# Performance work log

Measured on AMD Instinct MI355X. Metric: run time of the kernel, lower is better.

## Reference

```python
import jax, jax.numpy as jnp
import numpy as np

N_HEAD = 16
N_KV = 4
HEAD_DIM = 128
EPS = 1e-6


def setup_inputs() -> dict:
    key = jax.random.key(0)
    k1, k2, k3 = jax.random.split(key, 3)
    d_model = N_HEAD * HEAD_DIM
    qkv_out = (N_HEAD + 2 * N_KV) * HEAD_DIM
    B, T = 2, 2048
    x = jax.random.normal(k1, (B, T, d_model), dtype=jnp.float32)
    W_qkv = jax.random.normal(k2, (d_model, qkv_out), dtype=jnp.float32) * (d_model ** -0.5)
    W_proj = jax.random.normal(k3, (d_model, d_model), dtype=jnp.float32) * (d_model ** -0.5)
    q_scale = jnp.ones((HEAD_DIM,), dtype=jnp.float32)
    k_scale = jnp.ones((HEAD_DIM,), dtype=jnp.float32)
    return {"x": x, "W_qkv": W_qkv, "W_proj": W_proj, "q_scale": q_scale, "k_scale": k_scale}


def _rms_norm(t):
    return t * jax.lax.rsqrt(jnp.mean(t * t, axis=-1, keepdims=True) + EPS)


def reference(x, W_qkv, W_proj, q_scale, k_scale):
    B, T, C = x.shape
    qkv = x @ W_qkv  # [B, T, (H+2*KV)*D]
    q, k, v = jnp.split(qkv, [N_HEAD * HEAD_DIM, (N_HEAD + N_KV) * HEAD_DIM], axis=-1)
    q = q.reshape(B, T, N_HEAD, HEAD_DIM).transpose(0, 2, 1, 3)  # [B,H,T,D]
    k = k.reshape(B, T, N_KV, HEAD_DIM).transpose(0, 2, 1, 3)    # [B,KV,T,D]
    v = v.reshape(B, T, N_KV, HEAD_DIM).transpose(0, 2, 1, 3)
    # QK RMS-norm with learned per-dim scales
    q = _rms_norm(q) * q_scale
    k = _rms_norm(k) * k_scale
    # GQA: repeat kv heads to match query heads
    rep = N_HEAD // N_KV
    k = jnp.repeat(k, rep, axis=1)
    v = jnp.repeat(v, rep, axis=1)
    # causal SDPA
    scale = 1.0 / jnp.sqrt(jnp.float32(HEAD_DIM))
    scores = jnp.einsum('bhqd,bhkd->bhqk', q, k) * scale
    causal = jnp.tril(jnp.ones((T, T), dtype=bool))
    scores = jnp.where(causal, scores, jnp.finfo(scores.dtype).min)
    attn = jax.nn.softmax(scores, axis=-1)
    y = jnp.einsum('bhqk,bhkd->bhqd', attn, v)  # [B,H,T,D]
    y = y.transpose(0, 2, 1, 3).reshape(B, T, C)
    return y @ W_proj
```

## Files before the change

kernel.cpp:

```cpp
#include <hip/hip_runtime.h>

typedef __bf16 bf16;
typedef __bf16 bf16x8 __attribute__((ext_vector_type(8)));
typedef __bf16 bf16x4 __attribute__((ext_vector_type(4)));
typedef float f32x4 __attribute__((ext_vector_type(4)));
typedef float f32x16 __attribute__((ext_vector_type(16)));
typedef unsigned u32x4 __attribute__((ext_vector_type(4)));

#define EXP2F(x) __builtin_amdgcn_exp2f(x)

#define LOAD_LDS16(gp, lp)                                                     \
  __builtin_amdgcn_global_load_lds(                                            \
      (const __attribute__((address_space(1))) void*)(gp),                     \
      (__attribute__((address_space(3))) void*)(lp), 16, 0, 0)

__global__ __launch_bounds__(256) void k_cvt_x(const float* __restrict__ in,
                                               bf16* __restrict__ out, int n4) {
  int i = blockIdx.x * 256 + threadIdx.x;
  if (i < n4) {
    float4 v = ((const float4*)in)[i];
    bf16x4 o = {(bf16)v.x, (bf16)v.y, (bf16)v.z, (bf16)v.w};
    ((bf16x4*)out)[i] = o;
  }
}

__global__ __launch_bounds__(256) void k_transpose(const float* __restrict__ in,
                                                   bf16* __restrict__ out,
                                                   int R, int C) {
  __shared__ bf16 t[64 * 65];
  int tid = threadIdx.x;
  int c0 = blockIdx.x * 64, r0 = blockIdx.y * 64;
#pragma unroll
  for (int i = 0; i < 16; ++i) {
    int f = i * 256 + tid;
    int rl = f >> 6, cl = f & 63;
    t[rl * 65 + cl] = (bf16)in[(size_t)(r0 + rl) * C + c0 + cl];
  }
  __syncthreads();
#pragma unroll
  for (int i = 0; i < 16; ++i) {
    int f = i * 256 + tid;
    int cl = f >> 6, rl = f & 63;
    out[(size_t)(c0 + cl) * R + r0 + rl] = t[rl * 65 + cl];
  }
}

template <typename OutT>
__global__ __launch_bounds__(512, 2) void k_gemm256(const bf16* __restrict__ A,
                                                    const bf16* __restrict__ Bt,
                                                    OutT* __restrict__ C,
                                                    int M, int N, int K) {
  __shared__ alignas(16) bf16 As[2][2][4 * 256 * 8];
  __shared__ alignas(16) bf16 Bs[2][2][4 * 256 * 8];
  int tid = threadIdx.x;
  int wid = tid >> 6, lane = tid & 63;
  int g = lane >> 4, lr = lane & 15;
  int wrow = (wid >> 2) * 128, wcol = (wid & 3) * 64;
  int row0 = blockIdx.x * 256, col0 = blockIdx.y * 256;
  int NT = K >> 6;
  f32x4 acc[8][4] = {};

  auto stageA = [&](int buf, int kh, int kt) {
#pragma unroll
    for (int pass = 0; pass < 2; ++pass) {
      int slot = pass * 512 + tid;
      int kseg = slot >> 8, row = slot & 255;
      LOAD_LDS16(A + (size_t)(row0 + row) * K + kt * 64 + kh * 32 + kseg * 8,
                 &As[buf][kh][slot * 8]);
    }
  };
  auto stageB = [&](int buf, int kh, int kt) {
#pragma unroll
    for (int pass = 0; pass < 2; ++pass) {
      int slot = pass * 512 + tid;
      int kseg = slot >> 8, row = slot & 255;
      LOAD_LDS16(Bt + (size_t)(col0 + row) * K + kt * 64 + kh * 32 + kseg * 8,
                 &Bs[buf][kh][slot * 8]);
    }
  };
  auto dsA = [&](int buf, int s, int mq, bf16x8* af) {
#pragma unroll
    for (int i = 0; i < 4; ++i)
      af[i] = *(const bf16x8*)&As[buf][s]
                  [((g << 8) + wrow + (mq * 4 + i) * 16 + lr) * 8];
  };
  auto dsB = [&](int buf, int s, bf16x8* bfr) {
#pragma unroll
    for (int i = 0; i < 4; ++i)
      bfr[i] = *(const bf16x8*)&Bs[buf][s][((g << 8) + wcol + i * 16 + lr) * 8];
  };
  auto mfma16 = [&](int mq, bf16x8* af, bf16x8* bfr) {
    __builtin_amdgcn_s_setprio(1);
#pragma unroll
    for (int i = 0; i < 4; ++i)
#pragma unroll
      for (int n = 0; n < 4; ++n)
        acc[mq * 4 + i][n] = __builtin_amdgcn_mfma_f32_16x16x32_bf16(
            af[i], bfr[n], acc[mq * 4 + i][n], 0, 0, 0);
    __builtin_amdgcn_s_setprio(0);
  };

  stageA(0, 0, 0);
  stageB(0, 0, 0);
  stageA(0, 1, 0);
  stageB(0, 1, 0);
  asm volatile("s_waitcnt vmcnt(4)" ::: "memory");
  __builtin_amdgcn_s_barrier();

  for (int T = 0; T < NT; ++T) {
    int buf = T & 1, nbuf = buf ^ 1;
    bool more = (T + 1 < NT);
    bf16x8 af[4], bfr[4];
    dsA(buf, 0, 0, af);
    dsB(buf, 0, bfr);
    if (more) stageA(nbuf, 0, T + 1);
    __builtin_amdgcn_sched_barrier(0);
    __builtin_amdgcn_s_barrier();
    asm volatile("s_waitcnt lgkmcnt(0)" ::: "memory");
    __builtin_amdgcn_sched_barrier(0);
    mfma16(0, af, bfr);
    __builtin_amdgcn_s_barrier();
    dsA(buf, 0, 1, af);
    if (more) {
      stageB(nbuf, 0, T + 1);
      asm volatile("s_waitcnt vmcnt(4)" ::: "memory");
    } else {
      asm volatile("s_waitcnt vmcnt(0)" ::: "memory");
    }
    __builtin_amdgcn_sched_barrier(0);
    __builtin_amdgcn_s_barrier();
    asm volatile("s_waitcnt lgkmcnt(0)" ::: "memory");
    __builtin_amdgcn_sched_barrier(0);
    mfma16(1, af, bfr);
    __builtin_amdgcn_s_barrier();
    dsA(buf, 1, 0, af);
    dsB(buf, 1, bfr);
    if (more) stageA(nbuf, 1, T + 1);
    __builtin_amdgcn_sched_barrier(0);
    __builtin_amdgcn_s_barrier();
    asm volatile("s_waitcnt lgkmcnt(0)" ::: "memory");
    __builtin_amdgcn_sched_barrier(0);
    mfma16(0, af, bfr);
    __builtin_amdgcn_s_barrier();
    dsA(buf, 1, 1, af);
    if (more) {
      stageB(nbuf, 1, T + 1);
      asm volatile("s_waitcnt vmcnt(4)" ::: "memory");
    }
    __builtin_amdgcn_sched_barrier(0);
    __builtin_amdgcn_s_barrier();
    asm volatile("s_waitcnt lgkmcnt(0)" ::: "memory");
    __builtin_amdgcn_sched_barrier(0);
    mfma16(1, af, bfr);
    __builtin_amdgcn_s_barrier();
  }

#pragma unroll
  for (int mi = 0; mi < 8; ++mi)
#pragma unroll
    for (int ni = 0; ni < 4; ++ni) {
      int rb = row0 + wrow + mi * 16 + g * 4;
      int cc = col0 + wcol + ni * 16 + lr;
#pragma unroll
      for (int r = 0; r < 4; ++r) {
        float v = acc[mi][ni][r];
        C[(size_t)(rb + r) * N + cc] = (OutT)v;
      }
    }
}

__global__ __launch_bounds__(256) void k_qknorm(bf16* __restrict__ qkv,
                                                const float* __restrict__ qs,
                                                const float* __restrict__ ks) {
  int tok = blockIdx.x;
  int wid = threadIdx.x >> 6, lane = threadIdx.x & 63;
  int d = lane * 2;
  bf16* rowp = qkv + (size_t)tok * 3072;
#pragma unroll
  for (int i = 0; i < 5; ++i) {
    int cb = (i < 4) ? (wid + i * 4) * 128 : 2048 + wid * 128;
    float v0 = (float)rowp[cb + d], v1 = (float)rowp[cb + d + 1];
    float ss = v0 * v0 + v1 * v1;
#pragma unroll
    for (int off = 1; off < 64; off <<= 1) ss += __shfl_xor(ss, off);
    float r = rsqrtf(ss * (1.0f / 128.0f) + 1e-6f);
    float s0, s1, extra;
    if (i < 4) {
      s0 = qs[d]; s1 = qs[d + 1];
      extra = 0.08838834764831845f * 1.4426950408889634f;
    } else {
      s0 = ks[d]; s1 = ks[d + 1]; extra = 1.0f;
    }
    rowp[cb + d] = (bf16)(v0 * r * s0 * extra);
    rowp[cb + d + 1] = (bf16)(v1 * r * s1 * extra);
  }
}

__global__ __launch_bounds__(256) void k_vt(const bf16* __restrict__ qkv,
                                            bf16* __restrict__ Vt) {
  __shared__ bf16 t[64 * 65];
  int tid = threadIdx.x;
  int t0 = blockIdx.x * 64, d0 = blockIdx.y * 64;
  int bh = blockIdx.z;
  int b = bh >> 2, kvh = bh & 3;
  const bf16* src = qkv + (size_t)(b * 2048) * 3072 + 2560 + kvh * 128;
  bf16* dst = Vt + (size_t)bh * 128 * 2048;
#pragma unroll
  for (int i = 0; i < 16; ++i) {
    int f = i * 256 + tid;
    int tl = f >> 6, dl = f & 63;
    t[tl * 65 + dl] = src[(size_t)(t0 + tl) * 3072 + d0 + dl];
  }
  __syncthreads();
#pragma unroll
  for (int i = 0; i < 16; ++i) {
    int f = i * 256 + tid;
    int dl = f >> 6, tl = f & 63;
    dst[(size_t)(d0 + dl) * 2048 + t0 + tl] = t[tl * 65 + dl];
  }
}

__device__ inline unsigned pack2bf(float a, float b) {
  union { bf16 h[2]; unsigned u; } x;
  x.h[0] = (bf16)a;
  x.h[1] = (bf16)b;
  return x.u;
}

__global__ __launch_bounds__(256, 2) void k_attn(const bf16* __restrict__ qkv,
                                                 const bf16* __restrict__ Vt,
                                                 bf16* __restrict__ y) {
  int qt = gridDim.x - 1 - blockIdx.x;
  int h = blockIdx.y, b = blockIdx.z;
  int kvh = h >> 2;
  int tid = threadIdx.x;
  int wid = tid >> 6, lane = tid & 63;
  int qc = lane & 31, hi = lane >> 5;
  __shared__ alignas(16) bf16 Ks[2][16 * 64 * 8];
  __shared__ alignas(16) bf16 Vs[2][128 * 64];
  const bf16* Qb = qkv + (size_t)(b * 2048) * 3072 + h * 128;
  const bf16* Kb = qkv + (size_t)(b * 2048) * 3072 + 2048 + kvh * 128;
  const bf16* Vb = Vt + (size_t)(b * 4 + kvh) * 128 * 2048;
  int qw0 = qt * 128 + wid * 32;
  int qg = qw0 + qc;
  bf16x8 qf[8];
#pragma unroll
  for (int s = 0; s < 8; ++s)
    qf[s] = *(const bf16x8*)&Qb[(size_t)qg * 3072 + s * 16 + hi * 8];
  f32x16 acc[4] = {};
  float mrun = -1e30f, lrun = 0.f;

  auto STAGE = [&](int buf, int kt2) {
    int s0 = kt2 * 64;
#pragma unroll
    for (int i = 0; i < 4; ++i) {
      int slot = i * 256 + tid;
      int ch = slot >> 6, row = slot & 63;
      LOAD_LDS16(Kb + (size_t)(s0 + row) * 3072 + ch * 8, &Ks[buf][slot * 8]);
    }
#pragma unroll
    for (int i = 0; i < 4; ++i) {
      int slot = i * 256 + tid;
      int d = slot >> 3, c = slot & 7;
      LOAD_LDS16(Vb + (size_t)d * 2048 + s0 + ((c ^ (d & 7)) * 8),
                 &Vs[buf][slot * 8]);
    }
  };

  STAGE(0, 0);
  int cur = 0;
  int ktmax = 2 * qt + 1;
  for (int kt = 0; kt <= ktmax; ++kt) {
    int s0 = kt * 64;
    if (kt < ktmax) {
      STAGE(cur ^ 1, kt + 1);
      asm volatile("s_waitcnt vmcnt(8)" ::: "memory");
    } else {
      asm volatile("s_waitcnt vmcnt(0)" ::: "memory");
    }
    __builtin_amdgcn_s_barrier();
    __builtin_amdgcn_sched_barrier(0);
    if (s0 <= qw0 + 31) {
      f32x16 sc[2] = {};
#pragma unroll
      for (int s = 0; s < 8; ++s)
#pragma unroll
        for (int n = 0; n < 2; ++n) {
          bf16x8 kf =
              *(const bf16x8*)&Ks[cur][(((2 * s + hi) << 6) + n * 32 + qc) * 8];
          sc[n] =
              __builtin_amdgcn_mfma_f32_32x32x16_bf16(kf, qf[s], sc[n], 0, 0, 0);
        }
      if (s0 + 63 > qw0) {
#pragma unroll
        for (int n = 0; n < 2; ++n)
#pragma unroll
          for (int r = 0; r < 16; ++r) {
            int kg = s0 + n * 32 + (r & 3) + 8 * (r >> 2) + 4 * hi;
            if (kg > qg) sc[n][r] = -1e30f;
          }
      }
      float pm = -1e30f;
#pragma unroll
      for (int n = 0; n < 2; ++n)
#pragma unroll
        for (int r = 0; r < 16; ++r) pm = fmaxf(pm, sc[n][r]);
      pm = fmaxf(pm, __shfl_xor(pm, 32));
      if (__any(pm > mrun + 11.0f)) {
        float mnew = fmaxf(mrun, pm);
        float scl = EXP2F(mrun - mnew);
        mrun = mnew;
        lrun *= scl;
        float sv[16];
#pragma unroll
        for (int r = 0; r < 16; ++r)
          sv[r] = __shfl(scl, (r & 3) + 8 * (r >> 2) + 4 * hi);
#pragma unroll
        for (int dt = 0; dt < 4; ++dt)
#pragma unroll
          for (int r = 0; r < 16; ++r) acc[dt][r] *= sv[r];
      }
      float rs = 0.f;
#pragma unroll
      for (int n = 0; n < 2; ++n) {
        unsigned pk[8];
#pragma unroll
        for (int mm = 0; mm < 8; ++mm) {
          float e0 = EXP2F(sc[n][2 * mm] - mrun);
          float e1 = EXP2F(sc[n][2 * mm + 1] - mrun);
          rs += e0 + e1;
          pk[mm] = pack2bf(e0, e1);
        }
#pragma unroll
        for (int l2 = 0; l2 < 2; ++l2) {
          unsigned a0 = pk[4 * l2 + 0], b0 = pk[4 * l2 + 2];
          unsigned a1 = pk[4 * l2 + 1], b1 = pk[4 * l2 + 3];
          asm volatile("v_permlane32_swap_b32 %0, %1" : "+v"(a0), "+v"(b0));
          asm volatile("v_permlane32_swap_b32 %0, %1" : "+v"(a1), "+v"(b1));
          u32x4 w = {a0, a1, b0, b1};
          bf16x8 pf = __builtin_bit_cast(bf16x8, w);
          int ksg = 2 * n + l2;
#pragma unroll
          for (int dt = 0; dt < 4; ++dt) {
            int drow = dt * 32 + qc;
            bf16x8 vf = *(const bf16x8*)&Vs[cur][(drow * 8 +
                                                  ((2 * ksg + hi) ^ (qc & 7))) *
                                                 8];
            acc[dt] =
                __builtin_amdgcn_mfma_f32_32x32x16_bf16(pf, vf, acc[dt], 0, 0, 0);
          }
        }
      }
      rs += __shfl_xor(rs, 32);
      lrun += rs;
    }
    __builtin_amdgcn_s_barrier();
    cur ^= 1;
  }
  float rlv = 1.0f / lrun;
  float rcl[16];
#pragma unroll
  for (int r = 0; r < 16; ++r)
    rcl[r] = __shfl(rlv, (r & 3) + 8 * (r >> 2) + 4 * hi);
#pragma unroll
  for (int dt = 0; dt < 4; ++dt)
#pragma unroll
    for (int r = 0; r < 16; ++r) {
      int row = qw0 + (r & 3) + 8 * (r >> 2) + 4 * hi;
      float v = acc[dt][r] * rcl[r];
      y[(size_t)(b * 2048 + row) * 2048 + h * 128 + dt * 32 + qc] = (bf16)v;
    }
}

extern "C" void kernel_launch(void* const* d_in, const int* in_sizes, int n_in,
                              void* d_out, int out_size, void* d_ws,
                              size_t ws_size, hipStream_t stream) {
  const float* x = (const float*)d_in[0];
  const float* Wqkv = (const float*)d_in[1];
  const float* Wproj = (const float*)d_in[2];
  const float* qs = (const float*)d_in[3];
  const float* ks = (const float*)d_in[4];
  float* out = (float*)d_out;
  char* ws = (char*)d_ws;

  bf16* xb = (bf16*)(ws);
  bf16* Wqkvt = (bf16*)(ws + (size_t)(16u << 20));
  bf16* Wprojt = (bf16*)(ws + (size_t)(28u << 20));
  bf16* qkv = (bf16*)(ws + (size_t)(36u << 20));
  bf16* Vt = Wqkvt;
  bf16* y = xb;

  k_cvt_x<<<8192, 256, 0, stream>>>(x, xb, 8388608 / 4);
  k_transpose<<<dim3(3072 / 64, 2048 / 64), 256, 0, stream>>>(Wqkv, Wqkvt, 2048, 3072);
  k_transpose<<<dim3(2048 / 64, 2048 / 64), 256, 0, stream>>>(Wproj, Wprojt, 2048, 2048);
  k_gemm256<bf16><<<dim3(16, 12), 512, 0, stream>>>(xb, Wqkvt, qkv, 4096, 3072, 2048);
  k_qknorm<<<4096, 256, 0, stream>>>(qkv, qs, ks);
  k_vt<<<dim3(32, 2, 8), 256, 0, stream>>>(qkv, Vt);
  k_attn<<<dim3(16, 16, 2), 256, 0, stream>>>(qkv, Vt, y);
  k_gemm256<float><<<dim3(16, 8), 512, 0, stream>>>(y, Wprojt, out, 4096, 2048, 2048);
}
```

Before: 275.3 us.

## Use 128-row GEMM tiles for output projection and read V directly from global in attention

Templates the GEMM on the M tile size and launches the output projection with 128-row tiles, giving 256 blocks instead of 128 for better CU coverage. In the attention kernel it drops the LDS staging of V and loads V fragments straight from global memory, which frees LDS and lets occupancy rise to 4 blocks per CU. The direct V reads give up LDS reuse and the swizzled layout, so more global and L2 traffic and latency are exposed inside the PV MFMA loop.

```diff
diff --git a/kernel.cpp b/kernel.cpp
--- a/kernel.cpp
+++ b/kernel.cpp
@@ -45,26 +45,30 @@
   }
 }
 
-template <typename OutT>
+template <typename OutT, int BM>
 __global__ __launch_bounds__(512, 2) void k_gemm256(const bf16* __restrict__ A,
                                                     const bf16* __restrict__ Bt,
                                                     OutT* __restrict__ C,
                                                     int M, int N, int K) {
-  __shared__ alignas(16) bf16 As[2][2][4 * 256 * 8];
+  constexpr int ASZ = 4 * BM * 8;
+  constexpr int MREP = BM / 32;
+  __shared__ alignas(16) bf16 As[2][2][ASZ];
   __shared__ alignas(16) bf16 Bs[2][2][4 * 256 * 8];
   int tid = threadIdx.x;
   int wid = tid >> 6, lane = tid & 63;
   int g = lane >> 4, lr = lane & 15;
-  int wrow = (wid >> 2) * 128, wcol = (wid & 3) * 64;
-  int row0 = blockIdx.x * 256, col0 = blockIdx.y * 256;
+  int wrow = (wid >> 2) * (BM / 2), wcol = (wid & 3) * 64;
+  int row0 = blockIdx.x * BM, col0 = blockIdx.y * 256;
   int NT = K >> 6;
-  f32x4 acc[8][4] = {};
+  f32x4 acc[MREP][4] = {};
 
   auto stageA = [&](int buf, int kh, int kt) {
 #pragma unroll
-    for (int pass = 0; pass < 2; ++pass) {
+    for (int pass = 0; pass < BM / 128; ++pass) {
       int slot = pass * 512 + tid;
-      int kseg = slot >> 8, row = slot & 255;
+      int kseg, row;
+      if constexpr (BM == 256) { kseg = slot >> 8; row = slot & 255; }
+      else { kseg = slot >> 7; row = slot & 127; }
       LOAD_LDS16(A + (size_t)(row0 + row) * K + kt * 64 + kh * 32 + kseg * 8,
                  &As[buf][kh][slot * 8]);
     }
@@ -82,7 +86,7 @@
 #pragma unroll
     for (int i = 0; i < 4; ++i)
       af[i] = *(const bf16x8*)&As[buf][s]
-                  [((g << 8) + wrow + (mq * 4 + i) * 16 + lr) * 8];
+                  [(g * BM + wrow + (mq * 4 + i) * 16 + lr) * 8];
   };
   auto dsB = [&](int buf, int s, bf16x8* bfr) {
 #pragma unroll
@@ -104,59 +108,93 @@
   stageB(0, 0, 0);
   stageA(0, 1, 0);
   stageB(0, 1, 0);
-  asm volatile("s_waitcnt vmcnt(4)" ::: "memory");
+  if constexpr (BM == 256)
+    asm volatile("s_waitcnt vmcnt(4)" ::: "memory");
+  else
+    asm volatile("s_waitcnt vmcnt(3)" ::: "memory");
   __builtin_amdgcn_s_barrier();
 
   for (int T = 0; T < NT; ++T) {
     int buf = T & 1, nbuf = buf ^ 1;
     bool more = (T + 1 < NT);
     bf16x8 af[4], bfr[4];
-    dsA(buf, 0, 0, af);
-    dsB(buf, 0, bfr);
-    if (more) stageA(nbuf, 0, T + 1);
-    __builtin_amdgcn_sched_barrier(0);
-    __builtin_amdgcn_s_barrier();
-    asm volatile("s_waitcnt lgkmcnt(0)" ::: "memory");
-    __builtin_amdgcn_sched_barrier(0);
-    mfma16(0, af, bfr);
-    __builtin_amdgcn_s_barrier();
-    dsA(buf, 0, 1, af);
-    if (more) {
-      stageB(nbuf, 0, T + 1);
-      asm volatile("s_waitcnt vmcnt(4)" ::: "memory");
+    if constexpr (BM == 256) {
+      dsA(buf, 0, 0, af);
+      dsB(buf, 0, bfr);
+      if (more) stageA(nbuf, 0, T + 1);
+      __builtin_amdgcn_sched_barrier(0);
+      __builtin_amdgcn_s_barrier();
+      asm volatile("s_waitcnt lgkmcnt(0)" ::: "memory");
+      __builtin_amdgcn_sched_barrier(0);
+      mfma16(0, af, bfr);
+      __builtin_amdgcn_s_barrier();
+      dsA(buf, 0, 1, af);
+      if (more) {
+        stageB(nbuf, 0, T + 1);
+        asm volatile("s_waitcnt vmcnt(4)" ::: "memory");
+      } else {
+        asm volatile("s_waitcnt vmcnt(0)" ::: "memory");
+      }
+      __builtin_amdgcn_sched_barrier(0);
+      __builtin_amdgcn_s_barrier();
+      asm volatile("s_waitcnt lgkmcnt(0)" ::: "memory");
+      __builtin_amdgcn_sched_barrier(0);
+      mfma16(1, af, bfr);
+      __builtin_amdgcn_s_barrier();
+      dsA(buf, 1, 0, af);
+      dsB(buf, 1, bfr);
+      if (more) stageA(nbuf, 1, T + 1);
+      __builtin_amdgcn_sched_barrier(0);
+      __builtin_amdgcn_s_barrier();
+      asm volatile("s_waitcnt lgkmcnt(0)" ::: "memory");
+      __builtin_amdgcn_sched_barrier(0);
+      mfma16(0, af, bfr);
+      __builtin_amdgcn_s_barrier();
+      dsA(buf, 1, 1, af);
+      if (more) {
+        stageB(nbuf, 1, T + 1);
+        asm volatile("s_waitcnt vmcnt(4)" ::: "memory");
+      }
+      __builtin_amdgcn_sched_barrier(0);
+      __builtin_amdgcn_s_barrier();
+      asm volatile("s_waitcnt lgkmcnt(0)" ::: "memory");
+      __builtin_amdgcn_sched_barrier(0);
+      mfma16(1, af, bfr);
+      __builtin_amdgcn_s_barrier();
     } else {
-      asm volatile("s_waitcnt vmcnt(0)" ::: "memory");
-    }
-    __builtin_amdgcn_sched_barrier(0);
-    __builtin_amdgcn_s_barrier();
-    asm volatile("s_waitcnt lgkmcnt(0)" ::: "memory");
-    __builtin_amdgcn_sched_barrier(0);
-    mfma16(1, af, bfr);
-    __builtin_amdgcn_s_barrier();
-    dsA(buf, 1, 0, af);
-    dsB(buf, 1, bfr);
-    if (more) stageA(nbuf, 1, T + 1);
-    __builtin_amdgcn_sched_barrier(0);
-    __builtin_amdgcn_s_barrier();
-    asm volatile("s_waitcnt lgkmcnt(0)" ::: "memory");
-    __builtin_amdgcn_sched_barrier(0);
-    mfma16(0, af, bfr);
-    __builtin_amdgcn_s_barrier();
-    dsA(buf, 1, 1, af);
-    if (more) {
-      stageB(nbuf, 1, T + 1);
-      asm volatile("s_waitcnt vmcnt(4)" ::: "memory");
-    }
-    __builtin_amdgcn_sched_barrier(0);
-    __builtin_amdgcn_s_barrier();
-    asm volatile("s_waitcnt lgkmcnt(0)" ::: "memory");
-    __builtin_amdgcn_sched_barrier(0);
-    mfma16(1, af, bfr);
-    __builtin_amdgcn_s_barrier();
-  }
-
-#pragma unroll
-  for (int mi = 0; mi < 8; ++mi)
+      dsA(buf, 0, 0, af);
+      dsB(buf, 0, bfr);
+      if (more) {
+        stageA(nbuf, 0, T + 1);
+        stageB(nbuf, 0, T + 1);
+        asm volatile("s_waitcnt vmcnt(3)" ::: "memory");
+      } else {
+        asm volatile("s_waitcnt vmcnt(0)" ::: "memory");
+      }
+      __builtin_amdgcn_sched_barrier(0);
+      __builtin_amdgcn_s_barrier();
+      asm volatile("s_waitcnt lgkmcnt(0)" ::: "memory");
+      __builtin_amdgcn_sched_barrier(0);
+      mfma16(0, af, bfr);
+      __builtin_amdgcn_s_barrier();
+      dsA(buf, 1, 0, af);
+      dsB(buf, 1, bfr);
+      if (more) {
+        stageA(nbuf, 1, T + 1);
+        stageB(nbuf, 1, T + 1);
+        asm volatile("s_waitcnt vmcnt(3)" ::: "memory");
+      }
+      __builtin_amdgcn_sched_barrier(0);
+      __builtin_amdgcn_s_barrier();
+      asm volatile("s_waitcnt lgkmcnt(0)" ::: "memory");
+      __builtin_amdgcn_sched_barrier(0);
+      mfma16(0, af, bfr);
+      __builtin_amdgcn_s_barrier();
+    }
+  }
+
+#pragma unroll
+  for (int mi = 0; mi < MREP; ++mi)
 #pragma unroll
     for (int ni = 0; ni < 4; ++ni) {
       int rb = row0 + wrow + mi * 16 + g * 4;
@@ -227,7 +265,7 @@
   return x.u;
 }
 
-__global__ __launch_bounds__(256, 2) void k_attn(const bf16* __restrict__ qkv,
+__global__ __launch_bounds__(256, 4) void k_attn(const bf16* __restrict__ qkv,
                                                  const bf16* __restrict__ Vt,
                                                  bf16* __restrict__ y) {
   int qt = gridDim.x - 1 - blockIdx.x;
@@ -237,7 +275,6 @@
   int wid = tid >> 6, lane = tid & 63;
   int qc = lane & 31, hi = lane >> 5;
   __shared__ alignas(16) bf16 Ks[2][16 * 64 * 8];
-  __shared__ alignas(16) bf16 Vs[2][128 * 64];
   const bf16* Qb = qkv + (size_t)(b * 2048) * 3072 + h * 128;
   const bf16* Kb = qkv + (size_t)(b * 2048) * 3072 + 2048 + kvh * 128;
   const bf16* Vb = Vt + (size_t)(b * 4 + kvh) * 128 * 2048;
@@ -257,13 +294,6 @@
       int slot = i * 256 + tid;
       int ch = slot >> 6, row = slot & 63;
       LOAD_LDS16(Kb + (size_t)(s0 + row) * 3072 + ch * 8, &Ks[buf][slot * 8]);
-    }
-#pragma unroll
-    for (int i = 0; i < 4; ++i) {
-      int slot = i * 256 + tid;
-      int d = slot >> 3, c = slot & 7;
-      LOAD_LDS16(Vb + (size_t)d * 2048 + s0 + ((c ^ (d & 7)) * 8),
-                 &Vs[buf][slot * 8]);
     }
   };
 
@@ -274,7 +304,7 @@
     int s0 = kt * 64;
     if (kt < ktmax) {
       STAGE(cur ^ 1, kt + 1);
-      asm volatile("s_waitcnt vmcnt(8)" ::: "memory");
+      asm volatile("s_waitcnt vmcnt(4)" ::: "memory");
     } else {
       asm volatile("s_waitcnt vmcnt(0)" ::: "memory");
     }
@@ -342,10 +372,8 @@
           int ksg = 2 * n + l2;
 #pragma unroll
           for (int dt = 0; dt < 4; ++dt) {
-            int drow = dt * 32 + qc;
-            bf16x8 vf = *(const bf16x8*)&Vs[cur][(drow * 8 +
-                                                  ((2 * ksg + hi) ^ (qc & 7))) *
-                                                 8];
+            bf16x8 vf = *(const bf16x8*)&Vb[(size_t)(dt * 32 + qc) * 2048 + s0 +
+                                            (2 * ksg + hi) * 8];
             acc[dt] =
                 __builtin_amdgcn_mfma_f32_32x32x16_bf16(pf, vf, acc[dt], 0, 0, 0);
           }
@@ -393,9 +421,9 @@
   k_cvt_x<<<8192, 256, 0, stream>>>(x, xb, 8388608 / 4);
   k_transpose<<<dim3(3072 / 64, 2048 / 64), 256, 0, stream>>>(Wqkv, Wqkvt, 2048, 3072);
   k_transpose<<<dim3(2048 / 64, 2048 / 64), 256, 0, stream>>>(Wproj, Wprojt, 2048, 2048);
-  k_gemm256<bf16><<<dim3(16, 12), 512, 0, stream>>>(xb, Wqkvt, qkv, 4096, 3072, 2048);
+  k_gemm256<bf16, 256><<<dim3(16, 12), 512, 0, stream>>>(xb, Wqkvt, qkv, 4096, 3072, 2048);
   k_qknorm<<<4096, 256, 0, stream>>>(qkv, qs, ks);
   k_vt<<<dim3(32, 2, 8), 256, 0, stream>>>(qkv, Vt);
   k_attn<<<dim3(16, 16, 2), 256, 0, stream>>>(qkv, Vt, y);
-  k_gemm256<float><<<dim3(16, 8), 512, 0, stream>>>(y, Wprojt, out, 4096, 2048, 2048);
-}
+  k_gemm256<float, 128><<<dim3(32, 8), 512, 0, stream>>>(y, Wprojt, out, 4096, 2048, 2048);
+}
```

Result: slower. 427.4 us (+55.2%).
